# Optimization experiments

Hardware: AMD Instinct MI355X
Metric: run time of the kernel (lower is better)

Reference implementation:

```python
import jax, jax.numpy as jnp
import numpy as np

NUM_HEADS = 8
H_DIM = 24
COORDS_DIM = 3
NUM_W_PER_DIST = 8
BLOCK_SIZE = 128
N_HASHES = 3
N = 32768
HASH_DIM = H_DIM + (COORDS_DIM - 1) + 2  # q/k augmented with RPE coordinate terms


def layernorm(x, g, b, eps=1e-5):
    mu = x.mean(-1, keepdims=True)
    var = ((x - mu) ** 2).mean(-1, keepdims=True)
    return (x - mu) * jax.lax.rsqrt(var + eps) * g + b


def setup_inputs() -> dict:
    key = jax.random.key(0)
    ks = jax.random.split(key, 16)
    d, H = H_DIM, NUM_HEADS
    s = lambda i, shape, scale: jax.random.normal(ks[i], shape, jnp.float32) * scale
    return {
        "x": s(0, (N, d), 1.0),
        "coords": jax.random.uniform(ks[1], (N, COORDS_DIM), jnp.float32),
        "norm1_g": jnp.ones((d,), jnp.float32),
        "norm1_b": jnp.zeros((d,), jnp.float32),
        "Wq": s(2, (d, H * d), d ** -0.5),
        "Wk": s(3, (d, H * d), d ** -0.5),
        "Wv": s(4, (d, H * d), d ** -0.5),
        "w_rpe_W": s(5, (H * d, (COORDS_DIM - 1) * NUM_W_PER_DIST), 0.3),
        "Wo": s(6, (H * d, d), (H * d) ** -0.5),
        "bo": jnp.zeros((d,), jnp.float32),
        "norm2_g": jnp.ones((d,), jnp.float32),
        "norm2_b": jnp.zeros((d,), jnp.float32),
        "ff_W1": s(7, (d, d), d ** -0.5),
        "ff_b1": jnp.zeros((d,), jnp.float32),
        "ff_W2": s(8, (d, d), d ** -0.5),
        "ff_b2": jnp.zeros((d,), jnp.float32),
        "alphas": s(9, (N_HASHES, H, HASH_DIM), 1.0),  # E2LSH projection vectors
    }


def hept_attention(q, k, v, coords, w_rpe_W, alphas):
    # q,k,v: [n, H*d]. HEPT: fold RPE exp(-w*||dp||^2) into augmented q/k, then
    # n_hashes rounds of LSH sort + block-local attention, combined by softmax
    # over each round's log-normalizer (Reformer-style).
    n = q.shape[0]
    H, d, B = NUM_HEADS, H_DIM, BLOCK_SIZE
    nb = n // B
    q = q.reshape(n, H, d).transpose(1, 0, 2) * (d ** -0.5)  # [H,n,d]
    k = k.reshape(n, H, d).transpose(1, 0, 2)
    v = v.reshape(n, H, d).transpose(1, 0, 2)
    # per-head non-negative distance weights from w_rpe (mixture collapsed)
    Wm = w_rpe_W.reshape(H, d, COORDS_DIM - 1, NUM_W_PER_DIST)
    w = jnp.mean(Wm, axis=(1, 3)) ** 2                        # [H, c-1]
    p = coords[:, 1:]                                          # [n, c-1]
    sqn = jnp.einsum("hc,nc,nc->hn", w, p, p)                # w*||p||^2
    qp = jnp.sqrt(2.0) * jnp.sqrt(w)[:, None, :] * p[None]     # [H,n,c-1]
    ones = jnp.ones((H, n, 1), q.dtype)
    # q_hat.k_hat = q.k + 2*w*p_i.p_j - w|p_i|^2 - w|p_j|^2 = q.k - w*||p_i-p_j||^2
    q_hat = jnp.concatenate([q, qp, -sqn[..., None], ones], -1)  # [H,n,HASH_DIM]
    k_hat = jnp.concatenate([k, qp, ones, -sqn[..., None]], -1)
    outs, zs = [], []
    for r in range(N_HASHES):
        a = alphas[r]                                          # [H, HASH_DIM]
        iq = jnp.argsort(jnp.einsum("hne,he->hn", q_hat, a), -1)
        ik = jnp.argsort(jnp.einsum("hne,he->hn", k_hat, a), -1)
        qs = jnp.take_along_axis(q_hat, iq[..., None], 1).reshape(H, nb, B, -1)
        ks = jnp.take_along_axis(k_hat, ik[..., None], 1).reshape(H, nb, B, -1)
        vs = jnp.take_along_axis(v, ik[..., None], 1).reshape(H, nb, B, d)
        logits = jnp.einsum("hbqe,hbke->hbqk", qs, ks)         # [H,nb,B,B]
        z = jax.nn.logsumexp(logits, -1).reshape(H, n)
        o = jnp.einsum("hbqk,hbkd->hbqd", jax.nn.softmax(logits, -1), vs).reshape(H, n, d)
        inv = jnp.argsort(iq, -1)                              # unsort to input order
        outs.append(jnp.take_along_axis(o, inv[..., None], 1))
        zs.append(jnp.take_along_axis(z, inv, 1))
    wts = jax.nn.softmax(jnp.stack(zs), axis=0)[..., None]     # [R,H,n,1]
    out = (jnp.stack(outs) * wts).sum(0)                       # [H,n,d]
    return out.transpose(1, 0, 2).reshape(n, H * d)


def reference(x, coords, norm1_g, norm1_b, Wq, Wk, Wv, w_rpe_W, Wo, bo,
              norm2_g, norm2_b, ff_W1, ff_b1, ff_W2, ff_b2, alphas):
    xn = layernorm(x, norm1_g, norm1_b)
    q, k, v = xn @ Wq, xn @ Wk, xn @ Wv
    aggr = hept_attention(q, k, v, coords, w_rpe_W, alphas) @ Wo + bo
    x = x + aggr  # dropout is identity in eval mode
    h = layernorm(x, norm2_g, norm2_b)
    ff = jax.nn.relu(h @ ff_W1 + ff_b1) @ ff_W2 + ff_b2
    return x + ff
```

## Files before the change

### kernel.cpp

```cpp
#include <hip/hip_runtime.h>
#include <math.h>

#define NPT 32768
#define NH 8
#define HD 24
#define EDIM 28
#define NHASH 3
#define NSEG 48
#define NRH 24

typedef unsigned long long u64;
typedef unsigned short ushort;
typedef __attribute__((__vector_size__(8 * sizeof(short)))) short bf16x8;
typedef __attribute__((__vector_size__(4 * sizeof(float)))) float floatx4;
typedef __attribute__((__vector_size__(4 * sizeof(unsigned int)))) unsigned int uint32x4;

__device__ __forceinline__ ushort f2bf(float f) {
    unsigned u = __float_as_uint(f);
    unsigned r = u + 0x7FFF + ((u >> 16) & 1);
    return (ushort)(r >> 16);
}
__device__ __forceinline__ float us2f(ushort u) {
    return __uint_as_float(((unsigned)u) << 16);
}

__global__ __launch_bounds__(256) void k0b(
    const float* __restrict__ wrpe, const float* __restrict__ Wq,
    const float* __restrict__ Wk, const float* __restrict__ alphas,
    double* __restrict__ w64, double* __restrict__ cqp64,
    double* __restrict__ Aq, double* __restrict__ Ak, double* __restrict__ ct) {
    __shared__ double sw[16], sc[16];
    int t = threadIdx.x;
    if (t < 16) {
        int h = t >> 1, c = t & 1;
        double s = 0.0;
        for (int i = 0; i < 24; i++)
            for (int j = 0; j < 8; j++)
                s += (double)wrpe[(h * 24 + i) * 16 + c * 8 + j];
        double m = s / 192.0;
        sw[t] = m * m;
        sc[t] = sqrt(2.0) * fabs(m);
        w64[t] = sw[t];
        cqp64[t] = sc[t];
    }
    __syncthreads();
    const double QSCALE = 1.0 / sqrt(24.0);
    for (int idx = t; idx < 24 * NRH; idx += 256) {
        int i = idx / NRH, rh = idx % NRH;
        int h = rh & 7;
        double aq = 0.0, ak = 0.0;
        for (int e = 0; e < 24; e++) {
            double al = (double)alphas[rh * 28 + e];
            aq += (double)Wq[i * 192 + h * 24 + e] * al;
            ak += (double)Wk[i * 192 + h * 24 + e] * al;
        }
        Aq[idx] = aq * QSCALE;
        Ak[idx] = ak;
    }
    if (t < NRH) {
        int h = t & 7;
        ct[t * 4 + 0] = (double)alphas[t * 28 + 24] * sc[h * 2 + 0];
        ct[t * 4 + 1] = (double)alphas[t * 28 + 25] * sc[h * 2 + 1];
        ct[t * 4 + 2] = (double)alphas[t * 28 + 26];
        ct[t * 4 + 3] = (double)alphas[t * 28 + 27];
    }
}

__global__ __launch_bounds__(512) void k2s(
    const float* __restrict__ x, const float* __restrict__ n1g,
    const float* __restrict__ n1b, const float* __restrict__ coords,
    const double* __restrict__ Aq, const double* __restrict__ Ak,
    const double* __restrict__ ct, const double* __restrict__ w64,
    u64* __restrict__ keys, float* __restrict__ xnf) {
    __shared__ double sA[2][24][NRH];
    __shared__ double sCt[NRH][4];
    __shared__ double sW64[16];
    __shared__ double sGB[48];
    __shared__ double sXn[8][24];
    int t = threadIdx.x;
    for (int i = t; i < 24 * NRH; i += 512) sA[0][i / NRH][i % NRH] = Aq[i];
    for (int i = t; i < 24 * NRH; i += 512) sA[1][i / NRH][i % NRH] = Ak[i];
    for (int i = t; i < NRH * 4; i += 512) sCt[i / 4][i % 4] = ct[i];
    if (t < 16) sW64[t] = w64[t];
    if (t < 24) { sGB[t] = (double)n1g[t]; sGB[24 + t] = (double)n1b[t]; }
    __syncthreads();
    int wv = t >> 6, l = t & 63;
    for (int g = 0; g < 8; g++) {
        int n = blockIdx.x * 64 + g * 8 + wv;
        double xv = (l < 24) ? (double)x[(u64)n * 24 + l] : 0.0;
        double s = xv;
        s += __shfl_xor(s, 1); s += __shfl_xor(s, 2); s += __shfl_xor(s, 4);
        s += __shfl_xor(s, 8); s += __shfl_xor(s, 16);
        double mu = s / 24.0;
        double d = (l < 24) ? (xv - mu) : 0.0;
        double v2 = d * d;
        v2 += __shfl_xor(v2, 1); v2 += __shfl_xor(v2, 2); v2 += __shfl_xor(v2, 4);
        v2 += __shfl_xor(v2, 8); v2 += __shfl_xor(v2, 16);
        double rstd = 1.0 / sqrt(v2 / 24.0 + 1e-5);
        if (l < 24) {
            double xn = d * rstd * sGB[l] + sGB[24 + l];
            sXn[wv][l] = xn;
            xnf[(u64)n * 24 + l] = (float)xn;
        }
        double p0 = (double)coords[(u64)n * 3 + 1];
        double p1 = (double)coords[(u64)n * 3 + 2];
        if (l < 2 * NRH) {
            int qk = l / NRH, rh = l % NRH;
            int h = rh & 7;
            double sqn = sW64[2 * h] * p0 * p0 + sW64[2 * h + 1] * p1 * p1;
            double acc = sCt[rh][0] * p0 + sCt[rh][1] * p1;
            acc += qk ? (sCt[rh][2] - sqn * sCt[rh][3]) : (sCt[rh][3] - sqn * sCt[rh][2]);
            for (int i = 0; i < 24; i++) acc += sXn[wv][i] * sA[qk][i][rh];
            u64 u = (u64)__double_as_longlong(acc);
            if (u >> 63) u = ~u; else u |= 0x8000000000000000ULL;
            u64 key = (u & ~(u64)32767) | (u64)n;
            keys[(u64)l * NPT + n] = key;
        }
    }
}

__device__ __forceinline__ u64 shflx64(u64 v, int d) {
    int lo = __shfl_xor((int)(unsigned)v, d);
    int hi = __shfl_xor((int)(unsigned)(v >> 32), d);
    return ((u64)(unsigned)hi << 32) | (unsigned)lo;
}
__device__ __forceinline__ void cswap(u64& a, u64& b, bool up) {
    if ((a > b) == up) { u64 tmp = a; a = b; b = tmp; }
}
__device__ __forceinline__ u64* sslot(u64* s, int i) {
    int a = i << 3;
    a ^= ((a >> 9) & 7) << 4;
    return (u64*)((char*)s + a);
}
__device__ __forceinline__ void reg_passes(u64 e[8], int ib, int K, int jmax) {
    for (int j = jmax; j >= 1; j >>= 1) {
#pragma unroll
        for (int k = 0; k < 8; k++)
            if ((k & j) == 0) cswap(e[k], e[k | j], ((ib + k) & K) == 0);
    }
}
__device__ __forceinline__ void shfl_passes(u64 e[8], int t, int segoff, int K, int jhi, int jlo) {
    for (int j = jhi; j >= jlo; j >>= 1) {
        int d = j >> 3;
        bool lower = (t & d) == 0;
        bool up = ((segoff + ((t & ~d) << 3)) & K) == 0;
        bool keepmin = (lower == up);
#pragma unroll
        for (int k = 0; k < 8; k++) {
            u64 o = shflx64(e[k], d);
            bool ownsm = e[k] < o;
            e[k] = (ownsm == keepmin) ? e[k] : o;
        }
    }
}

#define K2P_PTS 32
#define INVLN2F 1.4426950408889634f
__global__ __launch_bounds__(1024) void k2p_sort(
    u64* keys,
    const float* __restrict__ xnf,
    const float* __restrict__ Wq, const float* __restrict__ Wk,
    const float* __restrict__ Wv, const float* __restrict__ coords,
    const double* __restrict__ w64, const double* __restrict__ cqp64,
    ushort* __restrict__ qhatB, ushort* __restrict__ khatB, ushort* __restrict__ varrB) {
    __shared__ __align__(16) char smem[65536];
    int t = threadIdx.x;
    if (blockIdx.x < 192) {
        u64* s = (u64*)smem;
        u64 gbase = (u64)blockIdx.x * 8192;
        int segoff = (int)(gbase & 32767);
        int ib = segoff + t * 8;
        u64 e[8];
#pragma unroll
        for (int k = 0; k < 8; k++) e[k] = keys[gbase + t * 8 + k];
        reg_passes(e, ib, 2, 1);
        reg_passes(e, ib, 4, 2);
        reg_passes(e, ib, 8, 4);
        for (int K = 16; K <= 512; K <<= 1) {
            shfl_passes(e, t, segoff, K, K >> 1, 8);
            reg_passes(e, ib, K, 4);
        }
#pragma unroll
        for (int k = 0; k < 8; k++) *sslot(s, t * 8 + k) = e[k];
        __syncthreads();
        for (int K = 1024; K <= 8192; K <<= 1) {
            for (int j = K >> 1; j >= 512; j >>= 1) {
                for (int p = t; p < 4096; p += 1024) {
                    int i = ((p & ~(j - 1)) << 1) | (p & (j - 1));
                    int i2 = i | j;
                    bool up = (((segoff + i) & K) == 0);
                    u64 a = *sslot(s, i), b = *sslot(s, i2);
                    if ((a > b) == up) { *sslot(s, i) = b; *sslot(s, i2) = a; }
                }
                __syncthreads();
            }
#pragma unroll
            for (int k = 0; k < 8; k++) e[k] = *sslot(s, t * 8 + k);
            shfl_passes(e, t, segoff, K, 256, 8);
            reg_passes(e, ib, K, 4);
            if (K < 8192) {
#pragma unroll
                for (int k = 0; k < 8; k++) *sslot(s, t * 8 + k) = e[k];
                __syncthreads();
            } else {
#pragma unroll
                for (int k = 0; k < 8; k++) keys[gbase + t * 8 + k] = e[k];
            }
        }
    } else {
        ushort* sT = (ushort*)smem;
        int n0 = (blockIdx.x - 192) * K2P_PTS;
        if (t < 576) {
            int m = t / 192, jj = t % 192;
            const float* W = (m == 0) ? Wq : ((m == 1) ? Wk : Wv);
            float wc[24];
#pragma unroll
            for (int i = 0; i < 24; i++) wc[i] = W[i * 192 + jj];
            const float scale = (m == 0) ? (float)(1.4426950408889634 / sqrt(24.0)) : 1.0f;
            int h = jj / 24, e = jj % 24;
            ushort* sbase = sT + ((m * 8 + h) * K2P_PTS) * 32 + e;
            for (int p = 0; p < K2P_PTS; p++) {
                int n = n0 + p;
                const float* xr = xnf + (u64)n * 24;
                float acc = 0.f;
#pragma unroll
                for (int i = 0; i < 24; i++) acc += xr[i] * wc[i];
                sbase[p * 32] = f2bf(acc * scale);
            }
        } else if (t < 640) {
            int l = t - 576;
            int h2 = l >> 3, e2 = 24 + (l & 7);
            double c0 = cqp64[h2 * 2], c1 = cqp64[h2 * 2 + 1];
            double wa = w64[h2 * 2], wb = w64[h2 * 2 + 1];
            ushort* qb = sT + ((0 * 8 + h2) * K2P_PTS) * 32 + e2;
            ushort* kb = sT + ((1 * 8 + h2) * K2P_PTS) * 32 + e2;
            ushort* vb = sT + ((2 * 8 + h2) * K2P_PTS) * 32 + e2;
            for (int p = 0; p < K2P_PTS; p++) {
                int n = n0 + p;
                double p0 = (double)coords[(u64)n * 3 + 1];
                double p1 = (double)coords[(u64)n * 3 + 2];
                float qv, kv;
                if (e2 < 26) {
                    int c = e2 - 24;
                    float qp = (float)((c ? c1 : c0) * (c ? p1 : p0));
                    qv = qp; kv = qp;
                } else if (e2 < 28) {
                    double sqn = wa * p0 * p0 + wb * p1 * p1;
                    if (e2 == 26) { qv = (float)(-sqn); kv = 1.0f; }
                    else          { qv = 1.0f; kv = (float)(-sqn); }
                } else {
                    qv = 0.0f; kv = 0.0f;
                }
                qb[p * 32] = f2bf(qv * INVLN2F);
                kb[p * 32] = f2bf(kv);
                vb[p * 32] = 0;
            }
        }
        __syncthreads();
        for (int c = t; c < 3 * 8 * K2P_PTS * 4; c += 1024) {
            int arrh = c >> 7, off = c & 127;
            int arr = arrh >> 3, hh = arrh & 7;
            uint32x4 v = *(const uint32x4*)(sT + arrh * (K2P_PTS * 32) + off * 8);
            ushort* op = (arr == 0) ? qhatB : ((arr == 1) ? khatB : varrB);
            *(uint32x4*)(op + (u64)hh * NPT * 32 + (u64)n0 * 32 + off * 8) = v;
        }
    }
}

__global__ __launch_bounds__(1024) void sort_tail1_fused(u64* keys) {
    __shared__ u64 s[8192];
    int t = threadIdx.x;
    u64 gbase = (u64)blockIdx.x * 8192;
    u64 pbase = gbase ^ 8192ULL;
    int ci = (int)((gbase >> 13) & 3);
    bool keepmin = (ci == 0) || (ci == 3);
    int segoff = (int)(gbase & 32767);
    int ib = segoff + t * 8;
    for (int i = t; i < 8192; i += 1024) {
        u64 a = keys[gbase + i];
        u64 b = keys[pbase + i];
        u64 mn = a < b ? a : b;
        u64 mx = a < b ? b : a;
        *sslot(s, i) = keepmin ? mn : mx;
    }
    __syncthreads();
    const int K = 16384;
    for (int j = 4096; j >= 512; j >>= 1) {
        for (int p = t; p < 4096; p += 1024) {
            int i = ((p & ~(j - 1)) << 1) | (p & (j - 1));
            int i2 = i | j;
            bool up = (((segoff + i) & K) == 0);
            u64 a = *sslot(s, i), b = *sslot(s, i2);
            if ((a > b) == up) { *sslot(s, i) = b; *sslot(s, i2) = a; }
        }
        __syncthreads();
    }
    u64 e[8];
#pragma unroll
    for (int k = 0; k < 8; k++) e[k] = *sslot(s, t * 8 + k);
    shfl_passes(e, t, segoff, K, 256, 8);
    reg_passes(e, ib, K, 4);
#pragma unroll
    for (int k = 0; k < 8; k++) keys[gbase + t * 8 + k] = e[k];
}

__device__ __forceinline__ int corank(int r, const u64* __restrict__ A,
                                      const u64* __restrict__ B) {
    int lo = r - 16384; if (lo < 0) lo = 0;
    int hi = r < 16384 ? r : 16384;
    while (lo < hi) {
        int a = (lo + hi + 1) >> 1;
        int b = r - a;
        u64 Bv = B[16383 - b];
        if (A[a - 1] < Bv) lo = a; else hi = a - 1;
    }
    return lo;
}
__global__ __launch_bounds__(128) void sort_corank(const u64* __restrict__ keys,
                                                   u64* __restrict__ keys2) {
    __shared__ int sh[2];
    int seg = blockIdx.x >> 8;
    int g = blockIdx.x & 255;
    const u64* A = keys + (u64)seg * 32768;
    const u64* B = A + 16384;
    int t = threadIdx.x;
    int r0 = g * 128;
    if (t == 0)  sh[0] = corank(r0, A, B);
    if (t == 64) sh[1] = corank(r0 + 128, A, B);
    __syncthreads();
    int aLo = sh[0], aHi = sh[1];
    int na = aHi - aLo;
    int bLo = r0 - aLo;
    u64 v;
    if (t < na) v = A[aLo + t];
    else        v = B[16383 - (bLo + (t - na))];
    keys2[(u64)seg * 32768 + r0 + t] = v;
}

__global__ __launch_bounds__(256, 4) void k3_attn(
    const u64* __restrict__ keys, const ushort* __restrict__ qhatB,
    const ushort* __restrict__ khatB, const ushort* __restrict__ varrB,
    ushort* __restrict__ ozB) {
    int rh3 = blockIdx.x % 24;
    int b = blockIdx.x / 24;
    int h = rh3 & 7, r = rh3 >> 3;
    __shared__ __align__(16) char smem[6144 + 32768 + 512];
    char* sVt = smem;
    char* sP  = smem + 6144;
    ushort* qidx = (ushort*)(smem + 6144 + 32768);
    ushort* kidx = qidx + 128;
    int t = threadIdx.x;
    int segQ = r * 8 + h, segK = 24 + r * 8 + h;
    if (t < 128) {
        qidx[t] = (ushort)(keys[(u64)segQ * NPT + b * 128 + t] & 32767ULL);
    } else {
        int i = t - 128;
        kidx[i] = (ushort)(keys[(u64)segK * NPT + b * 128 + i] & 32767ULL);
    }
    __syncthreads();

    int wave = t >> 6, L = t & 63;
    int quad = L >> 4, n16 = L & 15;

    const bf16x8* Qg = (const bf16x8*)(qhatB + (u64)h * NPT * 32);
    const bf16x8* Kg = (const bf16x8*)(khatB + (u64)h * NPT * 32);
    bf16x8 afr[2];
#pragma unroll
    for (int rtg = 0; rtg < 2; rtg++) {
        int qi = qidx[wave * 32 + rtg * 16 + n16];
        afr[rtg] = Qg[(u64)qi * 4 + quad];
    }
    bf16x8 bfr[8];
#pragma unroll
    for (int ct = 0; ct < 8; ct++) {
        int ki = kidx[ct * 16 + n16];
        bfr[ct] = Kg[(u64)ki * 4 + quad];
    }
    if (t < 128) {
        int ki = kidx[t];
        const bf16x8* vr = (const bf16x8*)(varrB + ((u64)h * NPT + ki) * 32);
        bf16x8 v0 = vr[0], v1 = vr[1], v2 = vr[2];
        int colb = ((t & 15) << 4) | ((t >> 4) << 1);
#pragma unroll
        for (int e = 0; e < 8; e++) {
            int e0 = e, e1 = 8 + e, e2 = 16 + e;
            *(short*)(sVt + e0 * 256 + (colb ^ ((e0 & 7) << 4))) = v0[e];
            *(short*)(sVt + e1 * 256 + (colb ^ ((e1 & 7) << 4))) = v1[e];
            *(short*)(sVt + e2 * 256 + (colb ^ ((e2 & 7) << 4))) = v2[e];
        }
    }
    __syncthreads();

    floatx4 acc[2][8];
#pragma unroll
    for (int rtg = 0; rtg < 2; rtg++)
#pragma unroll
        for (int ct = 0; ct < 8; ct++)
            acc[rtg][ct] = (floatx4){0.f, 0.f, 0.f, 0.f};
#pragma unroll
    for (int ct = 0; ct < 8; ct++) {
#pragma unroll
        for (int rtg = 0; rtg < 2; rtg++)
            acc[rtg][ct] = __builtin_amdgcn_mfma_f32_16x16x32_bf16(afr[rtg], bfr[ct], acc[rtg][ct], 0, 0, 0);
    }

    float mrow[2][4], srow[2][4];
#pragma unroll
    for (int rtg = 0; rtg < 2; rtg++) {
#pragma unroll
        for (int rg = 0; rg < 4; rg++) {
            float m = acc[rtg][0][rg];
#pragma unroll
            for (int ct = 1; ct < 8; ct++) m = fmaxf(m, acc[rtg][ct][rg]);
            m = fmaxf(m, __shfl_xor(m, 1));
            m = fmaxf(m, __shfl_xor(m, 2));
            m = fmaxf(m, __shfl_xor(m, 4));
            m = fmaxf(m, __shfl_xor(m, 8));
            mrow[rtg][rg] = m;
            float p[8];
            float s = 0.0f;
#pragma unroll
            for (int ct = 0; ct < 8; ct++) {
                p[ct] = exp2f(acc[rtg][ct][rg] - m);
                s += p[ct];
            }
            s += __shfl_xor(s, 1);
            s += __shfl_xor(s, 2);
            s += __shfl_xor(s, 4);
            s += __shfl_xor(s, 8);
            srow[rtg][rg] = s;
            unsigned w0, w1, w2, w3;
            asm("v_cvt_pk_bf16_f32 %0, %1, %2" : "=v"(w0) : "v"(p[0]), "v"(p[1]));
            asm("v_cvt_pk_bf16_f32 %0, %1, %2" : "=v"(w1) : "v"(p[2]), "v"(p[3]));
            asm("v_cvt_pk_bf16_f32 %0, %1, %2" : "=v"(w2) : "v"(p[4]), "v"(p[5]));
            asm("v_cvt_pk_bf16_f32 %0, %1, %2" : "=v"(w3) : "v"(p[6]), "v"(p[7]));
            int row = wave * 32 + rtg * 16 + quad * 4 + rg;
            uint32x4 pk = {w0, w1, w2, w3};
            *(uint32x4*)(sP + row * 256 + (((n16 << 4)) ^ ((row & 7) << 4))) = pk;
        }
    }

    floatx4 occ[2][2];
#pragma unroll
    for (int rtg = 0; rtg < 2; rtg++)
#pragma unroll
        for (int ct2 = 0; ct2 < 2; ct2++)
            occ[rtg][ct2] = (floatx4){0.f, 0.f, 0.f, 0.f};
#pragma unroll
    for (int ks = 0; ks < 4; ks++) {
        int kb = ks * 64 + quad * 16;
        bf16x8 bv[2], av[2];
#pragma unroll
        for (int ct2 = 0; ct2 < 2; ct2++) {
            int e = ct2 * 16 + n16;
            int ec = (e < 24) ? e : 0;
            bv[ct2] = *(const bf16x8*)(sVt + ec * 256 + (kb ^ ((ec & 7) << 4)));
        }
#pragma unroll
        for (int rtg = 0; rtg < 2; rtg++) {
            int rowA = wave * 32 + rtg * 16 + n16;
            av[rtg] = *(const bf16x8*)(sP + rowA * 256 + (kb ^ ((rowA & 7) << 4)));
        }
#pragma unroll
        for (int rtg = 0; rtg < 2; rtg++)
#pragma unroll
            for (int ct2 = 0; ct2 < 2; ct2++)
                occ[rtg][ct2] = __builtin_amdgcn_mfma_f32_16x16x32_bf16(av[rtg], bv[ct2], occ[rtg][ct2], 0, 0, 0);
    }

    const float LN2F = 0.6931471805599453f;
#pragma unroll
    for (int rtg = 0; rtg < 2; rtg++) {
#pragma unroll
        for (int rg = 0; rg < 4; rg++) {
            int row = wave * 32 + rtg * 16 + quad * 4 + rg;
            int oi = qidx[row];
            float inv = 1.0f / srow[rtg][rg];
            ushort* orow = ozB + ((u64)segQ * NPT + oi) * 32;
#pragma unroll
            for (int ct2 = 0; ct2 < 2; ct2++) {
                int col = ct2 * 16 + n16;
                if (col < 24) orow[col] = f2bf(occ[rtg][ct2][rg] * inv);
            }
            if (n16 == 0)
                *(float*)(orow + 24) = mrow[rtg][rg] * LN2F + __logf(srow[rtg][rg]);
        }
    }
}

#define K4PTS 32
#define AT_STR 196
#define W_STR 28
__global__ __launch_bounds__(256) void k4_final(
    const ushort* __restrict__ ozB,
    const float* __restrict__ x,
    const float* __restrict__ Wo, const float* __restrict__ bo,
    const float* __restrict__ g2, const float* __restrict__ b2,
    const float* __restrict__ W1, const float* __restrict__ b1f,
    const float* __restrict__ W2, const float* __restrict__ b2f,
    float* __restrict__ out) {
    __shared__ __align__(16) float sWoT[24][AT_STR];
    __shared__ __align__(16) float sW1T[24][W_STR], sW2T[24][W_STR];
    __shared__ float sB[5 * 24];
    __shared__ __align__(16) float attn[K4PTS][AT_STR];
    __shared__ float xrow[K4PTS][25];
    __shared__ __align__(16) float h2row[K4PTS][W_STR];
    __shared__ __align__(16) float ffrow[K4PTS][W_STR];
    int t = threadIdx.x;
    int base = blockIdx.x * K4PTS;
    for (int i = t; i < 4608; i += 256) sWoT[i % 24][i / 24] = Wo[i];
    for (int i = t; i < 576; i += 256) {
        sW1T[i % 24][i / 24] = W1[i];
        sW2T[i % 24][i / 24] = W2[i];
    }
    if (t < 24) {
        sB[t] = bo[t]; sB[24 + t] = g2[t]; sB[48 + t] = b2[t];
        sB[72 + t] = b1f[t]; sB[96 + t] = b2f[t];
    }
    if (t < K4PTS * 4) {
        int p = t >> 2, c = 24 + (t & 3);
        h2row[p][c] = 0.f; ffrow[p][c] = 0.f;
    }
    if (t < 24 * 4) {
        int rr = t >> 2, c = 24 + (t & 3);
        sW1T[rr][c] = 0.f; sW2T[rr][c] = 0.f;
    }
    {
        int p = t >> 3, h = t & 7;
        int n = base + p;
        const ushort* r0 = ozB + ((u64)(0 * 8 + h) * NPT + n) * 32;
        const ushort* r1 = ozB + ((u64)(1 * 8 + h) * NPT + n) * 32;
        const ushort* r2 = ozB + ((u64)(2 * 8 + h) * NPT + n) * 32;
        float z0 = *(const float*)(r0 + 24);
        float z1 = *(const float*)(r1 + 24);
        float z2 = *(const float*)(r2 + 24);
        float zm = fmaxf(z0, fmaxf(z1, z2));
        float e0 = __expf(z0 - zm), e1 = __expf(z1 - zm), e2 = __expf(z2 - zm);
        float inv = 1.0f / (e0 + e1 + e2);
        float w0 = e0 * inv, w1 = e1 * inv, w2 = e2 * inv;
#pragma unroll
        for (int e = 0; e < 24; e++)
            attn[p][h * 24 + e] = w0 * us2f(r0[e]) + w1 * us2f(r1[e]) + w2 * us2f(r2[e]);
    }
    __syncthreads();
    int p = t >> 3, oe = t & 7;
    int n = base + p;
    {
        const floatx4* ap = (const floatx4*)&attn[p][0];
        const floatx4* w0p = (const floatx4*)&sWoT[oe][0];
        const floatx4* w1p = (const floatx4*)&sWoT[oe + 8][0];
        const floatx4* w2p = (const floatx4*)&sWoT[oe + 16][0];
        floatx4 A0 = {0.f, 0.f, 0.f, 0.f}, A1 = A0, A2 = A0;
        for (int ii = 0; ii < 48; ii++) {
            floatx4 av = ap[ii];
            A0 += av * w0p[ii];
            A1 += av * w1p[ii];
            A2 += av * w2p[ii];
        }
        float a0 = A0[0] + A0[1] + A0[2] + A0[3];
        float a1 = A1[0] + A1[1] + A1[2] + A1[3];
        float a2 = A2[0] + A2[1] + A2[2] + A2[3];
        xrow[p][oe]      = x[n * 24 + oe]      + a0 + sB[oe];
        xrow[p][oe + 8]  = x[n * 24 + oe + 8]  + a1 + sB[oe + 8];
        xrow[p][oe + 16] = x[n * 24 + oe + 16] + a2 + sB[oe + 16];
    }
    float mu, rstd;
    {
        float s = xrow[p][oe] + xrow[p][oe + 8] + xrow[p][oe + 16];
        s += __shfl_xor(s, 1); s += __shfl_xor(s, 2); s += __shfl_xor(s, 4);
        mu = s / 24.0f;
        float v0 = xrow[p][oe] - mu, v1 = xrow[p][oe + 8] - mu, v2 = xrow[p][oe + 16] - mu;
        float v = v0 * v0 + v1 * v1 + v2 * v2;
        v += __shfl_xor(v, 1); v += __shfl_xor(v, 2); v += __shfl_xor(v, 4);
        rstd = 1.0f / sqrtf(v / 24.0f + 1e-5f);
    }
    h2row[p][oe]      = (xrow[p][oe] - mu)      * rstd * sB[24 + oe]      + sB[48 + oe];
    h2row[p][oe + 8]  = (xrow[p][oe + 8] - mu)  * rstd * sB[24 + oe + 8]  + sB[48 + oe + 8];
    h2row[p][oe + 16] = (xrow[p][oe + 16] - mu) * rstd * sB[24 + oe + 16] + sB[48 + oe + 16];
    {
        const floatx4* hp = (const floatx4*)&h2row[p][0];
        const floatx4* w0p = (const floatx4*)&sW1T[oe][0];
        const floatx4* w1p = (const floatx4*)&sW1T[oe + 8][0];
        const floatx4* w2p = (const floatx4*)&sW1T[oe + 16][0];
        floatx4 A0 = {0.f, 0.f, 0.f, 0.f}, A1 = A0, A2 = A0;
#pragma unroll
        for (int ii = 0; ii < 6; ii++) {
            floatx4 hv = hp[ii];
            A0 += hv * w0p[ii];
            A1 += hv * w1p[ii];
            A2 += hv * w2p[ii];
        }
        ffrow[p][oe]      = fmaxf(A0[0]+A0[1]+A0[2]+A0[3] + sB[72 + oe], 0.f);
        ffrow[p][oe + 8]  = fmaxf(A1[0]+A1[1]+A1[2]+A1[3] + sB[72 + oe + 8], 0.f);
        ffrow[p][oe + 16] = fmaxf(A2[0]+A2[1]+A2[2]+A2[3] + sB[72 + oe + 16], 0.f);
    }
    {
        const floatx4* fp = (const floatx4*)&ffrow[p][0];
        const floatx4* w0p = (const floatx4*)&sW2T[oe][0];
        const floatx4* w1p = (const floatx4*)&sW2T[oe + 8][0];
        const floatx4* w2p = (const floatx4*)&sW2T[oe + 16][0];
        floatx4 A0 = {0.f, 0.f, 0.f, 0.f}, A1 = A0, A2 = A0;
#pragma unroll
        for (int ii = 0; ii < 6; ii++) {
            floatx4 fv = fp[ii];
            A0 += fv * w0p[ii];
            A1 += fv * w1p[ii];
            A2 += fv * w2p[ii];
        }
        out[n * 24 + oe]      = xrow[p][oe]      + A0[0]+A0[1]+A0[2]+A0[3] + sB[96 + oe];
        out[n * 24 + oe + 8]  = xrow[p][oe + 8]  + A1[0]+A1[1]+A1[2]+A1[3] + sB[96 + oe + 8];
        out[n * 24 + oe + 16] = xrow[p][oe + 16] + A2[0]+A2[1]+A2[2]+A2[3] + sB[96 + oe + 16];
    }
}

extern "C" void kernel_launch(void* const* d_in, const int* in_sizes, int n_in,
                              void* d_out, int out_size, void* d_ws, size_t ws_size,
                              hipStream_t stream) {
    const float* x      = (const float*)d_in[0];
    const float* coords = (const float*)d_in[1];
    const float* n1g    = (const float*)d_in[2];
    const float* n1b    = (const float*)d_in[3];
    const float* Wq     = (const float*)d_in[4];
    const float* Wk     = (const float*)d_in[5];
    const float* Wv     = (const float*)d_in[6];
    const float* wrpe   = (const float*)d_in[7];
    const float* Wo     = (const float*)d_in[8];
    const float* bo     = (const float*)d_in[9];
    const float* n2g    = (const float*)d_in[10];
    const float* n2b    = (const float*)d_in[11];
    const float* W1     = (const float*)d_in[12];
    const float* b1     = (const float*)d_in[13];
    const float* W2     = (const float*)d_in[14];
    const float* b2     = (const float*)d_in[15];
    const float* alphas = (const float*)d_in[16];

    char* ws = (char*)d_ws;
    size_t off = 0;
    auto alloc = [&](size_t bytes) -> void* {
        void* p = ws + off;
        off = (off + bytes + 255) & ~(size_t)255;
        return p;
    };
    double* w64   = (double*)alloc(256);
    double* cqp   = (double*)alloc(256);
    double* Aq    = (double*)alloc(24 * NRH * 8);
    double* Ak    = (double*)alloc(24 * NRH * 8);
    double* ct    = (double*)alloc(NRH * 4 * 8);
    float*  xnf   = (float*)alloc((size_t)NPT * 24 * 4);
    ushort* qhatB = (ushort*)alloc((size_t)NH * NPT * 32 * 2);
    ushort* khatB = (ushort*)alloc((size_t)NH * NPT * 32 * 2);
    ushort* varrB = (ushort*)alloc((size_t)NH * NPT * 32 * 2);
    u64*    keys  = (u64*)alloc((size_t)NSEG * NPT * 8);
    u64*    keys2 = (u64*)alloc((size_t)NSEG * NPT * 8);
    ushort* ozB   = (ushort*)alloc((size_t)NHASH * NH * NPT * 32 * 2);
    if (off > ws_size) return;

    k0b<<<1, 256, 0, stream>>>(wrpe, Wq, Wk, alphas, w64, cqp, Aq, Ak, ct);
    k2s<<<NPT / 64, 512, 0, stream>>>(x, n1g, n1b, coords, Aq, Ak, ct, w64, keys, xnf);
    k2p_sort<<<192 + NPT / K2P_PTS, 1024, 0, stream>>>(keys, xnf, Wq, Wk, Wv, coords,
                                                       w64, cqp, qhatB, khatB, varrB);
    sort_tail1_fused<<<192, 1024, 0, stream>>>(keys);
    sort_corank<<<NSEG * 256, 128, 0, stream>>>(keys, keys2);
    k3_attn<<<256 * 8 * 3, 256, 0, stream>>>(keys2, qhatB, khatB, varrB, ozB);
    k4_final<<<NPT / K4PTS, 256, 0, stream>>>(ozB, x, Wo, bo, n2g, n2b,
                                              W1, b1, W2, b2, (float*)d_out);
}
```

Before: 292.3 us.

## Fuse final merge-path corank step into attention kernel, drop keys2 buffer

Removes the separate sort_corank kernel that merged two sorted halves into a keys2 buffer. Instead, each attention block computes the merge-path co-ranks for its own 128-row query and key windows and gathers the sorted indices directly from the half-sorted keys. This saves one kernel launch and a full read/write pass over the key array, at the cost of four serial binary searches at the start of every attention block. It also adds a min-blocks hint of 4 to k2p_sort's launch bounds.

```diff
diff --git a/kernel.cpp b/kernel.cpp
--- a/kernel.cpp
+++ b/kernel.cpp
@@ -156,7 +156,7 @@
 
 #define K2P_PTS 32
 #define INVLN2F 1.4426950408889634f
-__global__ __launch_bounds__(1024) void k2p_sort(
+__global__ __launch_bounds__(1024, 4) void k2p_sort(
     u64* keys,
     const float* __restrict__ xnf,
     const float* __restrict__ Wq, const float* __restrict__ Wk,
@@ -316,26 +316,6 @@
     }
     return lo;
 }
-__global__ __launch_bounds__(128) void sort_corank(const u64* __restrict__ keys,
-                                                   u64* __restrict__ keys2) {
-    __shared__ int sh[2];
-    int seg = blockIdx.x >> 8;
-    int g = blockIdx.x & 255;
-    const u64* A = keys + (u64)seg * 32768;
-    const u64* B = A + 16384;
-    int t = threadIdx.x;
-    int r0 = g * 128;
-    if (t == 0)  sh[0] = corank(r0, A, B);
-    if (t == 64) sh[1] = corank(r0 + 128, A, B);
-    __syncthreads();
-    int aLo = sh[0], aHi = sh[1];
-    int na = aHi - aLo;
-    int bLo = r0 - aLo;
-    u64 v;
-    if (t < na) v = A[aLo + t];
-    else        v = B[16383 - (bLo + (t - na))];
-    keys2[(u64)seg * 32768 + r0 + t] = v;
-}
 
 __global__ __launch_bounds__(256, 4) void k3_attn(
     const u64* __restrict__ keys, const ushort* __restrict__ qhatB,
@@ -344,18 +324,33 @@
     int rh3 = blockIdx.x % 24;
     int b = blockIdx.x / 24;
     int h = rh3 & 7, r = rh3 >> 3;
-    __shared__ __align__(16) char smem[6144 + 32768 + 512];
+    __shared__ __align__(16) char smem[6144 + 32768 + 512 + 16];
     char* sVt = smem;
     char* sP  = smem + 6144;
     ushort* qidx = (ushort*)(smem + 6144 + 32768);
     ushort* kidx = qidx + 128;
+    int* sh = (int*)(smem + 6144 + 32768 + 512);
     int t = threadIdx.x;
     int segQ = r * 8 + h, segK = 24 + r * 8 + h;
+    int r0 = b * 128;
+    const u64* AQ = keys + (u64)segQ * NPT;
+    const u64* BQ = AQ + 16384;
+    const u64* AK = keys + (u64)segK * NPT;
+    const u64* BK = AK + 16384;
+    if (t == 0)        sh[0] = corank(r0, AQ, BQ);
+    else if (t == 64)  sh[1] = corank(r0 + 128, AQ, BQ);
+    else if (t == 128) sh[2] = corank(r0, AK, BK);
+    else if (t == 192) sh[3] = corank(r0 + 128, AK, BK);
+    __syncthreads();
     if (t < 128) {
-        qidx[t] = (ushort)(keys[(u64)segQ * NPT + b * 128 + t] & 32767ULL);
+        int aLo = sh[0], na = sh[1] - aLo, bLo = r0 - aLo;
+        u64 v = (t < na) ? AQ[aLo + t] : BQ[16383 - (bLo + (t - na))];
+        qidx[t] = (ushort)(v & 32767ULL);
     } else {
         int i = t - 128;
-        kidx[i] = (ushort)(keys[(u64)segK * NPT + b * 128 + i] & 32767ULL);
+        int aLo = sh[2], na = sh[3] - aLo, bLo = r0 - aLo;
+        u64 v = (i < na) ? AK[aLo + i] : BK[16383 - (bLo + (i - na))];
+        kidx[i] = (ushort)(v & 32767ULL);
     }
     __syncthreads();
 
@@ -651,7 +646,6 @@
     ushort* khatB = (ushort*)alloc((size_t)NH * NPT * 32 * 2);
     ushort* varrB = (ushort*)alloc((size_t)NH * NPT * 32 * 2);
     u64*    keys  = (u64*)alloc((size_t)NSEG * NPT * 8);
-    u64*    keys2 = (u64*)alloc((size_t)NSEG * NPT * 8);
     ushort* ozB   = (ushort*)alloc((size_t)NHASH * NH * NPT * 32 * 2);
     if (off > ws_size) return;
 
@@ -660,8 +654,7 @@
     k2p_sort<<<192 + NPT / K2P_PTS, 1024, 0, stream>>>(keys, xnf, Wq, Wk, Wv, coords,
                                                        w64, cqp, qhatB, khatB, varrB);
     sort_tail1_fused<<<192, 1024, 0, stream>>>(keys);
-    sort_corank<<<NSEG * 256, 128, 0, stream>>>(keys, keys2);
-    k3_attn<<<256 * 8 * 3, 256, 0, stream>>>(keys2, qhatB, khatB, varrB, ozB);
+    k3_attn<<<256 * 8 * 3, 256, 0, stream>>>(keys, qhatB, khatB, varrB, ozB);
     k4_final<<<NPT / K4PTS, 256, 0, stream>>>(ozB, x, Wo, bo, n2g, n2b,
                                               W1, b1, W2, b2, (float*)d_out);
 }
```

Result: faster. 284.2 us (-2.8%).
